# Kernel optimization log

Hardware: AMD Instinct MI355X
Metric: run time of the kernel (lower is better)

Reference implementation:

```python
import jax, jax.numpy as jnp
import numpy as np

N, E, G = 20000, 320000, 64
IN_CH, HID, HEADS = 128, 64, 8
LEAKY_SLOPE = 0.2
SOFTMAX_EPS = 1e-16


def setup_inputs() -> dict:
    key = jax.random.key(0)
    ks = jax.random.split(key, 12)
    s = lambda fan_in: 1.0 / np.sqrt(fan_in)
    return {
        "x": jax.random.normal(ks[0], (N, IN_CH), jnp.float32),
        "edge_index": jax.random.randint(ks[1], (2, E), 0, N, jnp.int32),
        "batch": jnp.sort(jax.random.randint(ks[2], (N,), 0, G, jnp.int32)),
        "W1": jax.random.normal(ks[3], (HEADS * HID, IN_CH), jnp.float32) * s(IN_CH),
        "att_src1": jax.random.normal(ks[4], (HEADS, HID), jnp.float32) * s(HID),
        "att_dst1": jax.random.normal(ks[5], (HEADS, HID), jnp.float32) * s(HID),
        "b1": jnp.zeros((HEADS * HID,), jnp.float32),
        "W2": jax.random.normal(ks[6], (HID, HEADS * HID), jnp.float32) * s(HEADS * HID),
        "att_src2": jax.random.normal(ks[7], (1, HID), jnp.float32) * s(HID),
        "att_dst2": jax.random.normal(ks[8], (1, HID), jnp.float32) * s(HID),
        "b2": jnp.zeros((HID,), jnp.float32),
    }


def gat_conv(x, src, dst, W, att_src, att_dst, b):
    # x: [N, F_in]; W: [H*C, F_in]; att_*: [H, C]; b: [H*C]
    n = x.shape[0]
    heads, ch = att_src.shape
    h = (x @ W.T).reshape(n, heads, ch)                    # [N,H,C]
    a_s = jnp.einsum('nhc,hc->nh', h, att_src)             # [N,H]
    a_d = jnp.einsum('nhc,hc->nh', h, att_dst)             # [N,H]
    e = jax.nn.leaky_relu(a_s[src] + a_d[dst], LEAKY_SLOPE)  # [E,H]
    m = jax.ops.segment_max(e, dst, num_segments=n)        # scatter-softmax (stable)
    e = jnp.exp(e - m[dst])
    z = jax.ops.segment_sum(e, dst, num_segments=n)
    alpha = e / (z[dst] + SOFTMAX_EPS)                     # [E,H]
    msg = h[src] * alpha[:, :, None]                       # [E,H,C]
    out = jax.ops.segment_sum(msg, dst, num_segments=n)    # [N,H,C]
    return out.reshape(n, heads * ch) + b


def reference(x, edge_index, batch, W1, att_src1, att_dst1, b1, W2, att_src2, att_dst2, b2):
    # PyG GATConv default: add self loops
    loop = jnp.arange(N, dtype=edge_index.dtype)
    src = jnp.concatenate([edge_index[0], loop])
    dst = jnp.concatenate([edge_index[1], loop])

    x_mid = jax.nn.relu(gat_conv(x, src, dst, W1, att_src1, att_dst1, b1))  # [N, H*C]

    # global_mean_pool over `batch` segments
    sums = jax.ops.segment_sum(x_mid, batch, num_segments=G)
    cnt = jax.ops.segment_sum(jnp.ones((N,), x_mid.dtype), batch, num_segments=G)
    gat_mid_pooled = sums / jnp.maximum(cnt, 1.0)[:, None]                  # [G, H*C]

    # dropout identity in eval mode
    x_late = gat_conv(x_mid, src, dst, W2, att_src2, att_dst2, b2)          # [N, C]
    gat_late_view = x_late.reshape(-1, HEADS * HID)                          # [N/H, H*C]
    return gat_mid_pooled, gat_late_view
```

## Files before the change

kernel.cpp:

```cpp
#include <hip/hip_runtime.h>
#include <math.h>

#define NN 20000
#define EE 320000
#define ETOT 340000
#define GG 64
#define INCH 128
#define HIDC 64
#define NH 8
#define HC 512
#define SLOPE 0.2f
#define SMEPS 1e-16f

typedef unsigned short u16;
typedef unsigned int u32;
typedef __attribute__((ext_vector_type(8))) short bf16x8;
typedef __attribute__((ext_vector_type(4))) float f32x4;
typedef __attribute__((ext_vector_type(2))) float f32x2;

__device__ __forceinline__ float rlanef(float v, int l) {
  return __uint_as_float(__builtin_amdgcn_readlane(__float_as_uint(v), l));
}
__device__ __forceinline__ u16 f2bf(float f) {
  u32 x = __float_as_uint(f);
  x += 0x7FFFu + ((x >> 16) & 1u);
  return (u16)(x >> 16);
}
__device__ __forceinline__ float bflo(u32 w) { return __uint_as_float(w << 16); }
__device__ __forceinline__ float bfhi(u32 w) { return __uint_as_float(w & 0xffff0000u); }

#define PREP_B 10392
#define HIST_B 1329
__global__ void k_prep(const float* __restrict__ W1, const float* __restrict__ W2,
                       const float* __restrict__ as1, const float* __restrict__ ad1v,
                       const float* __restrict__ x, const int* __restrict__ ei,
                       u16* __restrict__ W1bf, u16* __restrict__ W2bf,
                       float* __restrict__ wB1, u16* __restrict__ xbf,
                       int* __restrict__ deg) {
  if (blockIdx.x >= PREP_B) {
    int i = (blockIdx.x - PREP_B) * 256 + threadIdx.x;
    if (i < ETOT) {
      int d = (i < EE) ? ei[EE + i] : (i - EE);
      atomicAdd(&deg[d], 1);
    }
    return;
  }
  int i = blockIdx.x * 256 + threadIdx.x;
  if (i < 65536) {
    W1bf[i] = f2bf(W1[i]);
  } else if (i < 65536 + 32768) {
    int j = i - 65536;
    W2bf[j] = f2bf(W2[j]);
  } else if (i < 65536 + 32768 + 2048) {
    int j = i - 65536 - 32768;
    int k = j >> 4, c = j & 15;
    int h = c & 7;
    const float* av = (c < 8) ? as1 : ad1v;
    float s = 0.f;
    for (int q = 0; q < 64; ++q) s += W1[(h * 64 + q) * 128 + k] * av[h * 64 + q];
    wB1[j] = s;
  } else {
    int j = i - 100352;
    if (j < NN * INCH) xbf[j] = f2bf(x[j]);
  }
}

__global__ __launch_bounds__(1024) void k_scan(const int* __restrict__ deg,
                                               int* __restrict__ rowstart) {
  __shared__ int wtot[16];
  int tid = threadIdx.x;
  int lane = tid & 63, w = tid >> 6;
  int base = tid * 20;
  int v[20];
  int s = 0;
#pragma unroll
  for (int k = 0; k < 20; ++k) {
    v[k] = (base + k < NN) ? deg[base + k] : 0;
    s += v[k];
  }
  int ps = s;
#pragma unroll
  for (int off = 1; off < 64; off <<= 1) {
    int t = __shfl_up(ps, off);
    if (lane >= off) ps += t;
  }
  if (lane == 63) wtot[w] = ps;
  __syncthreads();
  if (w == 0 && lane < 16) {
    int t = wtot[lane];
#pragma unroll
    for (int off = 1; off < 16; off <<= 1) {
      int u = __shfl_up(t, off);
      if (lane >= off) t += u;
    }
    wtot[lane] = t;
  }
  __syncthreads();
  int woff = (w == 0) ? 0 : wtot[w - 1];
  int run = woff + ps - s;
#pragma unroll
  for (int k = 0; k < 20; ++k) {
    run += v[k];
    if (base + k < NN) rowstart[base + k + 1] = run;
  }
  if (tid == 0) rowstart[0] = 0;
}

__global__ void k_fill(const int* __restrict__ ei, const int* __restrict__ rowstart,
                       int* __restrict__ wcur, int* __restrict__ csr) {
  int i = blockIdx.x * 256 + threadIdx.x;
  if (i >= ETOT) return;
  int s, d;
  if (i < EE) { s = ei[i]; d = ei[EE + i]; } else { s = i - EE; d = s; }
  int pos = rowstart[d] + atomicAdd(&wcur[d], 1);
  csr[pos] = s;
}

__global__ __launch_bounds__(256) void k_logits1(
    const float* __restrict__ x, const float* __restrict__ wB1,
    float* __restrict__ al1) {
  __shared__ float bs[128][16];
  int tid = threadIdx.x;
#pragma unroll
  for (int i = 0; i < 8; ++i) {
    int e = tid + i * 256;
    bs[e >> 4][e & 15] = wB1[e];
  }
  __syncthreads();
  int gt = blockIdx.x * 256 + tid;
  int r = gt >> 2; if (r > NN - 1) r = NN - 1;
  int q = gt & 3;
  const float* xp = x + (size_t)r * INCH;
  float acc[4] = {0.f, 0.f, 0.f, 0.f};
  for (int kq = 0; kq < 32; ++kq) {
    float4 a = *(const float4*)(xp + kq * 4);
    float av[4] = {a.x, a.y, a.z, a.w};
#pragma unroll
    for (int kk = 0; kk < 4; ++kk) {
      const float4 b = *(const float4*)&bs[kq * 4 + kk][q * 4];
      acc[0] = fmaf(av[kk], b.x, acc[0]);
      acc[1] = fmaf(av[kk], b.y, acc[1]);
      acc[2] = fmaf(av[kk], b.z, acc[2]);
      acc[3] = fmaf(av[kk], b.w, acc[3]);
    }
  }
  float4 o; o.x = acc[0]; o.y = acc[1]; o.z = acc[2]; o.w = acc[3];
  *(float4*)(al1 + (size_t)r * 16 + q * 4) = o;
}

__global__ __launch_bounds__(256) void k_agg1(
    const u16* __restrict__ xbf, const float* __restrict__ al1,
    const int* __restrict__ rowstart, const int* __restrict__ csr,
    u16* __restrict__ aggbf) {
  int n = blockIdx.x * 4 + (threadIdx.x >> 6);
  int lane = threadIdx.x & 63;
  int rs = __builtin_amdgcn_readfirstlane(rowstart[n]);
  int re = __builtin_amdgcn_readfirstlane(rowstart[n + 1]);
  float4 ad0 = *(const float4*)(al1 + (size_t)n * 16 + 8);
  float4 ad1 = *(const float4*)(al1 + (size_t)n * 16 + 12);
  float zp[NH] = {};
  f32x2 acc2[NH] = {};
  for (int base = rs; base < re; base += 64) {
    int cn = min(64, re - base);
    int idx = base + ((lane < cn) ? lane : 0);
    int s = csr[idx];
    float4 a0 = *(const float4*)(al1 + (size_t)s * 16);
    float4 a1 = *(const float4*)(al1 + (size_t)s * 16 + 4);
    float e[8] = {a0.x + ad0.x, a0.y + ad0.y, a0.z + ad0.z, a0.w + ad0.w,
                  a1.x + ad1.x, a1.y + ad1.y, a1.z + ad1.z, a1.w + ad1.w};
    float p[8];
#pragma unroll
    for (int h = 0; h < 8; ++h) {
      float t = e[h];
      t = fmaxf(t, SLOPE * t);
      float pv = __expf(t);
      pv = (lane < cn) ? pv : 0.f;
      p[h] = pv;
      zp[h] += pv;
    }
    int j = 0;
    for (; j + 3 < cn; j += 4) {
      int s0 = __builtin_amdgcn_readlane(s, j);
      int s1 = __builtin_amdgcn_readlane(s, j + 1);
      int s2 = __builtin_amdgcn_readlane(s, j + 2);
      int s3 = __builtin_amdgcn_readlane(s, j + 3);
      u32 x0 = *(const u32*)(xbf + (size_t)s0 * INCH + lane * 2);
      u32 x1 = *(const u32*)(xbf + (size_t)s1 * INCH + lane * 2);
      u32 x2 = *(const u32*)(xbf + (size_t)s2 * INCH + lane * 2);
      u32 x3 = *(const u32*)(xbf + (size_t)s3 * INCH + lane * 2);
      f32x2 v0; v0.x = bflo(x0); v0.y = bfhi(x0);
      f32x2 v1; v1.x = bflo(x1); v1.y = bfhi(x1);
      f32x2 v2; v2.x = bflo(x2); v2.y = bfhi(x2);
      f32x2 v3; v3.x = bflo(x3); v3.y = bfhi(x3);
#pragma unroll
      for (int h = 0; h < 8; ++h) {
        float p0 = rlanef(p[h], j);
        float p1 = rlanef(p[h], j + 1);
        float p2 = rlanef(p[h], j + 2);
        float p3 = rlanef(p[h], j + 3);
        f32x2 q0; q0.x = p0; q0.y = p0;
        f32x2 q1; q1.x = p1; q1.y = p1;
        f32x2 q2; q2.x = p2; q2.y = p2;
        f32x2 q3; q3.x = p3; q3.y = p3;
        acc2[h] = __builtin_elementwise_fma(q0, v0, acc2[h]);
        acc2[h] = __builtin_elementwise_fma(q1, v1, acc2[h]);
        acc2[h] = __builtin_elementwise_fma(q2, v2, acc2[h]);
        acc2[h] = __builtin_elementwise_fma(q3, v3, acc2[h]);
      }
    }
    for (; j < cn; ++j) {
      int sa = __builtin_amdgcn_readlane(s, j);
      u32 xa = *(const u32*)(xbf + (size_t)sa * INCH + lane * 2);
      f32x2 va; va.x = bflo(xa); va.y = bfhi(xa);
#pragma unroll
      for (int h = 0; h < 8; ++h) {
        float pa = rlanef(p[h], j);
        f32x2 pa2; pa2.x = pa; pa2.y = pa;
        acc2[h] = __builtin_elementwise_fma(pa2, va, acc2[h]);
      }
    }
  }
#pragma unroll
  for (int h = 0; h < 8; ++h) {
    float z = zp[h];
#pragma unroll
    for (int off = 32; off; off >>= 1) z += __shfl_xor(z, off);
    float inv = 1.f / (z + SMEPS);
    u32 pk = ((u32)f2bf(acc2[h].y * inv) << 16) | (u32)f2bf(acc2[h].x * inv);
    *(u32*)(aggbf + (size_t)h * NN * INCH + (size_t)n * INCH + lane * 2) = pk;
  }
}

__global__ __launch_bounds__(256) void k_gemm1h(
    const u16* __restrict__ aggbf, const u16* __restrict__ W1bf,
    const float* __restrict__ b1, u16* __restrict__ xmidbf) {
  int tid = threadIdx.x;
  int head = blockIdx.x & 7;
  int nb = blockIdx.x >> 3;
  int w = tid >> 6, l = tid & 63;
  int li = l & 15, hi = l >> 4;
  const u16* Ab = aggbf + (size_t)head * NN * INCH;
  const u16* Bb = W1bf + (size_t)head * 64 * INCH;

  bf16x8 Bf[4][4];
#pragma unroll
  for (int ks = 0; ks < 4; ++ks)
#pragma unroll
    for (int ct = 0; ct < 4; ++ct)
      Bf[ks][ct] = *(const bf16x8*)(Bb + (size_t)(ct * 16 + li) * INCH + ks * 32 + hi * 8);

  int nA = nb * 64 + w * 16 + li; if (nA > NN - 1) nA = NN - 1;
  const u16* Ap = Ab + (size_t)nA * INCH + hi * 8;
  f32x4 acc[4] = {};
#pragma unroll
  for (int ks = 0; ks < 4; ++ks) {
    bf16x8 Af = *(const bf16x8*)(Ap + ks * 32);
#pragma unroll
    for (int ct = 0; ct < 4; ++ct)
      acc[ct] = __builtin_amdgcn_mfma_f32_16x16x32_bf16(Af, Bf[ks][ct], acc[ct], 0, 0, 0);
  }
#pragma unroll
  for (int ct = 0; ct < 4; ++ct) {
    float bb = b1[head * 64 + ct * 16 + li];
#pragma unroll
    for (int reg = 0; reg < 4; ++reg) {
      int r = nb * 64 + w * 16 + hi * 4 + reg; if (r > NN - 1) r = NN - 1;
      float v = fmaxf(acc[ct][reg] + bb, 0.f);
      xmidbf[(size_t)r * HC + head * 64 + ct * 16 + li] = f2bf(v);
    }
  }
}

__global__ __launch_bounds__(256) void k_gemm2(
    const u16* __restrict__ xmb, const u16* __restrict__ W2bf,
    const float* __restrict__ atts, const float* __restrict__ attd,
    u16* __restrict__ h2bf, float* __restrict__ as2, float* __restrict__ ad2) {
  __shared__ float red[4][16][65];
  int tid = threadIdx.x;
  int w = tid >> 6, l = tid & 63;
  int li = l & 15, hi = l >> 4;
  int brow = blockIdx.x * 16;

  bf16x8 Bf[4][4];
#pragma unroll
  for (int ksl = 0; ksl < 4; ++ksl)
#pragma unroll
    for (int ct = 0; ct < 4; ++ct)
      Bf[ksl][ct] = *(const bf16x8*)(W2bf + (size_t)(ct * 16 + li) * HC + w * 128 + ksl * 32 + hi * 8);

  const u16* Ap = xmb + (size_t)(brow + li) * HC + w * 128 + hi * 8;
  f32x4 acc[4] = {};
#pragma unroll
  for (int ksl = 0; ksl < 4; ++ksl) {
    bf16x8 Af = *(const bf16x8*)(Ap + ksl * 32);
#pragma unroll
    for (int ct = 0; ct < 4; ++ct)
      acc[ct] = __builtin_amdgcn_mfma_f32_16x16x32_bf16(Af, Bf[ksl][ct], acc[ct], 0, 0, 0);
  }
#pragma unroll
  for (int ct = 0; ct < 4; ++ct)
#pragma unroll
    for (int reg = 0; reg < 4; ++reg)
      red[w][hi * 4 + reg][ct * 16 + li] = acc[ct][reg];
  __syncthreads();

  int c = l;
  float atv = atts[c], adv = attd[c];
  float vs[4], vd[4];
#pragma unroll
  for (int i = 0; i < 4; ++i) {
    int r = w + 4 * i;
    float v = red[0][r][c] + red[1][r][c] + red[2][r][c] + red[3][r][c];
    h2bf[(size_t)(brow + r) * HIDC + c] = f2bf(v);
    vs[i] = v * atv; vd[i] = v * adv;
  }
#pragma unroll
  for (int off = 32; off; off >>= 1) {
#pragma unroll
    for (int i = 0; i < 4; ++i) { vs[i] += __shfl_xor(vs[i], off); vd[i] += __shfl_xor(vd[i], off); }
  }
  if (l == 0) {
#pragma unroll
    for (int i = 0; i < 4; ++i) {
      int n = brow + w + 4 * i;
      as2[n] = vs[i]; ad2[n] = vd[i];
    }
  }
}

__global__ __launch_bounds__(256) void k_node2(
    const u16* __restrict__ h2bf, const float* __restrict__ as2, const float* __restrict__ ad2,
    const int* __restrict__ rowstart, const int* __restrict__ csr,
    const float* __restrict__ b2, float* __restrict__ out) {
  int n = blockIdx.x * 4 + (threadIdx.x >> 6);
  int lane = threadIdx.x & 63;
  int e = lane >> 4, c = lane & 15;
  int rs = __builtin_amdgcn_readfirstlane(rowstart[n]);
  int re = __builtin_amdgcn_readfirstlane(rowstart[n + 1]);
  float ad = ad2[n];
  f32x2 accA = {}, accB = {};
  float zp = 0.f;
  for (int base = rs; base < re; base += 8) {
    int iA = base + e, iB = base + 4 + e;
    bool okA = iA < re, okB = iB < re;
    int sA = csr[okA ? iA : re - 1];
    int sB = csr[okB ? iB : re - 1];
    float tA = as2[sA] + ad;
    float tB = as2[sB] + ad;
    const u32* hpA = (const u32*)(h2bf + (size_t)sA * HIDC + c * 4);
    const u32* hpB = (const u32*)(h2bf + (size_t)sB * HIDC + c * 4);
    u32 a0 = hpA[0], a1 = hpA[1];
    u32 b0 = hpB[0], b1 = hpB[1];
    tA = fmaxf(tA, SLOPE * tA);
    tB = fmaxf(tB, SLOPE * tB);
    float pA = okA ? __expf(tA) : 0.f;
    float pB = okB ? __expf(tB) : 0.f;
    zp += pA + pB;
    f32x2 vA0; vA0.x = bflo(a0); vA0.y = bfhi(a0);
    f32x2 vA1; vA1.x = bflo(a1); vA1.y = bfhi(a1);
    f32x2 vB0; vB0.x = bflo(b0); vB0.y = bfhi(b0);
    f32x2 vB1; vB1.x = bflo(b1); vB1.y = bfhi(b1);
    f32x2 pA2; pA2.x = pA; pA2.y = pA;
    f32x2 pB2; pB2.x = pB; pB2.y = pB;
    accA = __builtin_elementwise_fma(pA2, vA0, accA);
    accB = __builtin_elementwise_fma(pA2, vA1, accB);
    accA = __builtin_elementwise_fma(pB2, vB0, accA);
    accB = __builtin_elementwise_fma(pB2, vB1, accB);
  }
  float acc0 = accA.x, acc1 = accA.y, acc2v = accB.x, acc3 = accB.y;
  zp += __shfl_xor(zp, 16); zp += __shfl_xor(zp, 32);
  acc0 += __shfl_xor(acc0, 16); acc0 += __shfl_xor(acc0, 32);
  acc1 += __shfl_xor(acc1, 16); acc1 += __shfl_xor(acc1, 32);
  acc2v += __shfl_xor(acc2v, 16); acc2v += __shfl_xor(acc2v, 32);
  acc3 += __shfl_xor(acc3, 16); acc3 += __shfl_xor(acc3, 32);
  if (e == 0) {
    float inv = 1.f / (zp + SMEPS);
    float4 bv = *(const float4*)(b2 + c * 4);
    float4 o;
    o.x = acc0 * inv + bv.x; o.y = acc1 * inv + bv.y;
    o.z = acc2v * inv + bv.z; o.w = acc3 * inv + bv.w;
    *(float4*)(out + (size_t)n * HIDC + c * 4) = o;
  }
}

__device__ inline int lowerb(const int* a, int n, int v) {
  int lo = 0, hi = n;
  while (lo < hi) { int mid = (lo + hi) >> 1; if (a[mid] < v) lo = mid + 1; else hi = mid; }
  return lo;
}

__global__ __launch_bounds__(256) void k_pool(const u16* __restrict__ xmb,
                                              const int* __restrict__ batch,
                                              float* __restrict__ out) {
  __shared__ float red[4][128];
  int g = blockIdx.x >> 2;
  int cb = blockIdx.x & 3;
  int tid = threadIdx.x;
  int c2 = tid & 63;
  int rq = tid >> 6;
  int lo = lowerb(batch, NN, g);
  int hi = lowerb(batch, NN, g + 1);
  float sx = 0.f, sy = 0.f;
  for (int n = lo + rq; n < hi; n += 4) {
    u32 w = *(const u32*)(xmb + (size_t)n * HC + cb * 128 + c2 * 2);
    sx += bflo(w); sy += bfhi(w);
  }
  red[rq][c2 * 2] = sx; red[rq][c2 * 2 + 1] = sy;
  __syncthreads();
  if (rq == 0) {
    float inv = 1.f / fmaxf((float)(hi - lo), 1.f);
    float vx = red[0][c2 * 2] + red[1][c2 * 2] + red[2][c2 * 2] + red[3][c2 * 2];
    float vy = red[0][c2 * 2 + 1] + red[1][c2 * 2 + 1] + red[2][c2 * 2 + 1] + red[3][c2 * 2 + 1];
    float2 o; o.x = vx * inv; o.y = vy * inv;
    *(float2*)(out + (size_t)g * HC + cb * 128 + c2 * 2) = o;
  }
}

extern "C" void kernel_launch(void* const* d_in, const int* in_sizes, int n_in,
                              void* d_out, int out_size, void* d_ws, size_t ws_size,
                              hipStream_t stream) {
  const float* x     = (const float*)d_in[0];
  const int*   ei    = (const int*)d_in[1];
  const int*   batch = (const int*)d_in[2];
  const float* W1    = (const float*)d_in[3];
  const float* atts1 = (const float*)d_in[4];
  const float* attd1 = (const float*)d_in[5];
  const float* b1    = (const float*)d_in[6];
  const float* W2    = (const float*)d_in[7];
  const float* atts2 = (const float*)d_in[8];
  const float* attd2 = (const float*)d_in[9];
  const float* b2    = (const float*)d_in[10];
  float* out = (float*)d_out;

  float* ws = (float*)d_ws;
  size_t off = 0;
  u16*  aggbf  = (u16*)(ws + off); off += (size_t)NH * NN * INCH / 2;
  u16*  xmidbf = (u16*)(ws + off); off += (size_t)NN * HC / 2;
  u16*  h2bf   = (u16*)(ws + off); off += (size_t)NN * HIDC / 2;
  float* al1  = ws + off; off += (size_t)NN * 16;
  float* as2  = ws + off; off += NN;
  float* ad2  = ws + off; off += NN;
  u16*  W1bf  = (u16*)(ws + off); off += 65536 / 2;
  u16*  W2bf  = (u16*)(ws + off); off += 32768 / 2;
  float* wB1  = ws + off; off += 2048;
  u16*  xbf   = (u16*)(ws + off); off += (size_t)NN * INCH / 2;
  int* deg      = (int*)(ws + off); off += NN;
  int* wcur     = (int*)(ws + off); off += NN;
  int* rowstart = (int*)(ws + off); off += NN + 4;
  int* csr      = (int*)(ws + off); off += ETOT;

  hipMemsetAsync(deg, 0, sizeof(int) * 2 * NN, stream);
  k_prep<<<PREP_B + HIST_B, 256, 0, stream>>>(W1, W2, atts1, attd1, x, ei,
                                              W1bf, W2bf, wB1, xbf, deg);
  k_scan<<<1, 1024, 0, stream>>>(deg, rowstart);
  k_fill<<<(ETOT + 255) / 256, 256, 0, stream>>>(ei, rowstart, wcur, csr);

  k_logits1<<<313, 256, 0, stream>>>(x, wB1, al1);
  k_agg1<<<5000, 256, 0, stream>>>(xbf, al1, rowstart, csr, aggbf);
  k_gemm1h<<<313 * 8, 256, 0, stream>>>(aggbf, W1bf, b1, xmidbf);
  k_pool<<<GG * 4, 256, 0, stream>>>(xmidbf, batch, out);
  k_gemm2<<<1250, 256, 0, stream>>>(xmidbf, W2bf, atts2, attd2, h2bf, as2, ad2);
  k_node2<<<5000, 256, 0, stream>>>(h2bf, as2, ad2, rowstart, csr, b2, out + (size_t)GG * HC);
}
```

Measured before the change: 188.1 us.

## Merge fill with logits and pool with gemm2; stage attention weights in LDS

The CSR fill kernel and the layer-1 logits kernel become one launch, with the blocks split by index. The mean-pool kernel is likewise folded into the layer-2 GEMM launch. Together these remove two kernel launches and let the independent work overlap. In the aggregation kernel, per-edge attention weights are written to shared memory and read back as vectors instead of being broadcast with readlane; this trades scalar readlane traffic for LDS reads and extra shared memory per block, which may reduce occupancy.

```diff
diff --git a/kernel.cpp b/kernel.cpp
--- a/kernel.cpp
+++ b/kernel.cpp
@@ -18,9 +18,6 @@
 typedef __attribute__((ext_vector_type(4))) float f32x4;
 typedef __attribute__((ext_vector_type(2))) float f32x2;
 
-__device__ __forceinline__ float rlanef(float v, int l) {
-  return __uint_as_float(__builtin_amdgcn_readlane(__float_as_uint(v), l));
-}
 __device__ __forceinline__ u16 f2bf(float f) {
   u32 x = __float_as_uint(f);
   x += 0x7FFFu + ((x >> 16) & 1u);
@@ -106,28 +103,30 @@
   if (tid == 0) rowstart[0] = 0;
 }
 
-__global__ void k_fill(const int* __restrict__ ei, const int* __restrict__ rowstart,
-                       int* __restrict__ wcur, int* __restrict__ csr) {
-  int i = blockIdx.x * 256 + threadIdx.x;
-  if (i >= ETOT) return;
-  int s, d;
-  if (i < EE) { s = ei[i]; d = ei[EE + i]; } else { s = i - EE; d = s; }
-  int pos = rowstart[d] + atomicAdd(&wcur[d], 1);
-  csr[pos] = s;
-}
-
-__global__ __launch_bounds__(256) void k_logits1(
+#define FILL_B 1329
+__global__ __launch_bounds__(256) void k_fill_logits(
+    const int* __restrict__ ei, const int* __restrict__ rowstart,
+    int* __restrict__ wcur, int* __restrict__ csr,
     const float* __restrict__ x, const float* __restrict__ wB1,
     float* __restrict__ al1) {
   __shared__ float bs[128][16];
   int tid = threadIdx.x;
+  if (blockIdx.x < FILL_B) {
+    int i = blockIdx.x * 256 + tid;
+    if (i >= ETOT) return;
+    int s, d;
+    if (i < EE) { s = ei[i]; d = ei[EE + i]; } else { s = i - EE; d = s; }
+    int pos = rowstart[d] + atomicAdd(&wcur[d], 1);
+    csr[pos] = s;
+    return;
+  }
 #pragma unroll
   for (int i = 0; i < 8; ++i) {
     int e = tid + i * 256;
     bs[e >> 4][e & 15] = wB1[e];
   }
   __syncthreads();
-  int gt = blockIdx.x * 256 + tid;
+  int gt = (blockIdx.x - FILL_B) * 256 + tid;
   int r = gt >> 2; if (r > NN - 1) r = NN - 1;
   int q = gt & 3;
   const float* xp = x + (size_t)r * INCH;
@@ -148,11 +147,14 @@
   *(float4*)(al1 + (size_t)r * 16 + q * 4) = o;
 }
 
+#define PSTR 12
 __global__ __launch_bounds__(256) void k_agg1(
     const u16* __restrict__ xbf, const float* __restrict__ al1,
     const int* __restrict__ rowstart, const int* __restrict__ csr,
     u16* __restrict__ aggbf) {
-  int n = blockIdx.x * 4 + (threadIdx.x >> 6);
+  __shared__ float p_sh[4][64 * PSTR];
+  int wv = threadIdx.x >> 6;
+  int n = blockIdx.x * 4 + wv;
   int lane = threadIdx.x & 63;
   int rs = __builtin_amdgcn_readfirstlane(rowstart[n]);
   int re = __builtin_amdgcn_readfirstlane(rowstart[n + 1]);
@@ -160,6 +162,7 @@
   float4 ad1 = *(const float4*)(al1 + (size_t)n * 16 + 12);
   float zp[NH] = {};
   f32x2 acc2[NH] = {};
+  float* pw = &p_sh[wv][0];
   for (int base = rs; base < re; base += 64) {
     int cn = min(64, re - base);
     int idx = base + ((lane < cn) ? lane : 0);
@@ -177,6 +180,13 @@
       pv = (lane < cn) ? pv : 0.f;
       p[h] = pv;
       zp[h] += pv;
+    }
+    {
+      float* pd = pw + lane * PSTR;
+      f32x4 w0; w0.x = p[0]; w0.y = p[1]; w0.z = p[2]; w0.w = p[3];
+      f32x4 w1; w1.x = p[4]; w1.y = p[5]; w1.z = p[6]; w1.w = p[7];
+      *(f32x4*)(pd) = w0;
+      *(f32x4*)(pd + 4) = w1;
     }
     int j = 0;
     for (; j + 3 < cn; j += 4) {
@@ -188,35 +198,56 @@
       u32 x1 = *(const u32*)(xbf + (size_t)s1 * INCH + lane * 2);
       u32 x2 = *(const u32*)(xbf + (size_t)s2 * INCH + lane * 2);
       u32 x3 = *(const u32*)(xbf + (size_t)s3 * INCH + lane * 2);
+      f32x4 pA0 = *(const f32x4*)(pw + (j + 0) * PSTR);
+      f32x4 pA1 = *(const f32x4*)(pw + (j + 0) * PSTR + 4);
+      f32x4 pB0 = *(const f32x4*)(pw + (j + 1) * PSTR);
+      f32x4 pB1 = *(const f32x4*)(pw + (j + 1) * PSTR + 4);
+      f32x4 pC0 = *(const f32x4*)(pw + (j + 2) * PSTR);
+      f32x4 pC1 = *(const f32x4*)(pw + (j + 2) * PSTR + 4);
+      f32x4 pD0 = *(const f32x4*)(pw + (j + 3) * PSTR);
+      f32x4 pD1 = *(const f32x4*)(pw + (j + 3) * PSTR + 4);
       f32x2 v0; v0.x = bflo(x0); v0.y = bfhi(x0);
       f32x2 v1; v1.x = bflo(x1); v1.y = bfhi(x1);
       f32x2 v2; v2.x = bflo(x2); v2.y = bfhi(x2);
       f32x2 v3; v3.x = bflo(x3); v3.y = bfhi(x3);
 #pragma unroll
-      for (int h = 0; h < 8; ++h) {
-        float p0 = rlanef(p[h], j);
-        float p1 = rlanef(p[h], j + 1);
-        float p2 = rlanef(p[h], j + 2);
-        float p3 = rlanef(p[h], j + 3);
-        f32x2 q0; q0.x = p0; q0.y = p0;
-        f32x2 q1; q1.x = p1; q1.y = p1;
-        f32x2 q2; q2.x = p2; q2.y = p2;
-        f32x2 q3; q3.x = p3; q3.y = p3;
-        acc2[h] = __builtin_elementwise_fma(q0, v0, acc2[h]);
-        acc2[h] = __builtin_elementwise_fma(q1, v1, acc2[h]);
-        acc2[h] = __builtin_elementwise_fma(q2, v2, acc2[h]);
-        acc2[h] = __builtin_elementwise_fma(q3, v3, acc2[h]);
+      for (int h = 0; h < 4; ++h) {
+        f32x2 qA; qA.x = pA0[h]; qA.y = pA0[h];
+        f32x2 qB; qB.x = pB0[h]; qB.y = pB0[h];
+        f32x2 qC; qC.x = pC0[h]; qC.y = pC0[h];
+        f32x2 qD; qD.x = pD0[h]; qD.y = pD0[h];
+        acc2[h] = __builtin_elementwise_fma(qA, v0, acc2[h]);
+        acc2[h] = __builtin_elementwise_fma(qB, v1, acc2[h]);
+        acc2[h] = __builtin_elementwise_fma(qC, v2, acc2[h]);
+        acc2[h] = __builtin_elementwise_fma(qD, v3, acc2[h]);
+      }
+#pragma unroll
+      for (int h = 0; h < 4; ++h) {
+        f32x2 qA; qA.x = pA1[h]; qA.y = pA1[h];
+        f32x2 qB; qB.x = pB1[h]; qB.y = pB1[h];
+        f32x2 qC; qC.x = pC1[h]; qC.y = pC1[h];
+        f32x2 qD; qD.x = pD1[h]; qD.y = pD1[h];
+        acc2[4 + h] = __builtin_elementwise_fma(qA, v0, acc2[4 + h]);
+        acc2[4 + h] = __builtin_elementwise_fma(qB, v1, acc2[4 + h]);
+        acc2[4 + h] = __builtin_elementwise_fma(qC, v2, acc2[4 + h]);
+        acc2[4 + h] = __builtin_elementwise_fma(qD, v3, acc2[4 + h]);
       }
     }
     for (; j < cn; ++j) {
       int sa = __builtin_amdgcn_readlane(s, j);
       u32 xa = *(const u32*)(xbf + (size_t)sa * INCH + lane * 2);
+      f32x4 pA0 = *(const f32x4*)(pw + j * PSTR);
+      f32x4 pA1 = *(const f32x4*)(pw + j * PSTR + 4);
       f32x2 va; va.x = bflo(xa); va.y = bfhi(xa);
 #pragma unroll
-      for (int h = 0; h < 8; ++h) {
-        float pa = rlanef(p[h], j);
-        f32x2 pa2; pa2.x = pa; pa2.y = pa;
-        acc2[h] = __builtin_elementwise_fma(pa2, va, acc2[h]);
+      for (int h = 0; h < 4; ++h) {
+        f32x2 qA; qA.x = pA0[h]; qA.y = pA0[h];
+        acc2[h] = __builtin_elementwise_fma(qA, va, acc2[h]);
+      }
+#pragma unroll
+      for (int h = 0; h < 4; ++h) {
+        f32x2 qA; qA.x = pA1[h]; qA.y = pA1[h];
+        acc2[4 + h] = __builtin_elementwise_fma(qA, va, acc2[4 + h]);
       }
     }
   }
@@ -271,12 +302,45 @@
   }
 }
 
-__global__ __launch_bounds__(256) void k_gemm2(
+#define G2_B 1250
+__device__ inline int lowerb(const int* a, int n, int v) {
+  int lo = 0, hi = n;
+  while (lo < hi) { int mid = (lo + hi) >> 1; if (a[mid] < v) lo = mid + 1; else hi = mid; }
+  return lo;
+}
+
+__global__ __launch_bounds__(256) void k_gemm2_pool(
     const u16* __restrict__ xmb, const u16* __restrict__ W2bf,
     const float* __restrict__ atts, const float* __restrict__ attd,
-    u16* __restrict__ h2bf, float* __restrict__ as2, float* __restrict__ ad2) {
+    u16* __restrict__ h2bf, float* __restrict__ as2, float* __restrict__ ad2,
+    const int* __restrict__ batch, float* __restrict__ out) {
   __shared__ float red[4][16][65];
+  __shared__ float redp[4][128];
   int tid = threadIdx.x;
+  if (blockIdx.x >= G2_B) {
+    int bid = blockIdx.x - G2_B;
+    int g = bid >> 2;
+    int cb = bid & 3;
+    int c2 = tid & 63;
+    int rq = tid >> 6;
+    int lo = lowerb(batch, NN, g);
+    int hi = lowerb(batch, NN, g + 1);
+    float sx = 0.f, sy = 0.f;
+    for (int n = lo + rq; n < hi; n += 4) {
+      u32 w = *(const u32*)(xmb + (size_t)n * HC + cb * 128 + c2 * 2);
+      sx += bflo(w); sy += bfhi(w);
+    }
+    redp[rq][c2 * 2] = sx; redp[rq][c2 * 2 + 1] = sy;
+    __syncthreads();
+    if (rq == 0) {
+      float inv = 1.f / fmaxf((float)(hi - lo), 1.f);
+      float vx = redp[0][c2 * 2] + redp[1][c2 * 2] + redp[2][c2 * 2] + redp[3][c2 * 2];
+      float vy = redp[0][c2 * 2 + 1] + redp[1][c2 * 2 + 1] + redp[2][c2 * 2 + 1] + redp[3][c2 * 2 + 1];
+      float2 o; o.x = vx * inv; o.y = vy * inv;
+      *(float2*)(out + (size_t)g * HC + cb * 128 + c2 * 2) = o;
+    }
+    return;
+  }
   int w = tid >> 6, l = tid & 63;
   int li = l & 15, hi = l >> 4;
   int brow = blockIdx.x * 16;
@@ -383,39 +447,6 @@
   }
 }
 
-__device__ inline int lowerb(const int* a, int n, int v) {
-  int lo = 0, hi = n;
-  while (lo < hi) { int mid = (lo + hi) >> 1; if (a[mid] < v) lo = mid + 1; else hi = mid; }
-  return lo;
-}
-
-__global__ __launch_bounds__(256) void k_pool(const u16* __restrict__ xmb,
-                                              const int* __restrict__ batch,
-                                              float* __restrict__ out) {
-  __shared__ float red[4][128];
-  int g = blockIdx.x >> 2;
-  int cb = blockIdx.x & 3;
-  int tid = threadIdx.x;
-  int c2 = tid & 63;
-  int rq = tid >> 6;
-  int lo = lowerb(batch, NN, g);
-  int hi = lowerb(batch, NN, g + 1);
-  float sx = 0.f, sy = 0.f;
-  for (int n = lo + rq; n < hi; n += 4) {
-    u32 w = *(const u32*)(xmb + (size_t)n * HC + cb * 128 + c2 * 2);
-    sx += bflo(w); sy += bfhi(w);
-  }
-  red[rq][c2 * 2] = sx; red[rq][c2 * 2 + 1] = sy;
-  __syncthreads();
-  if (rq == 0) {
-    float inv = 1.f / fmaxf((float)(hi - lo), 1.f);
-    float vx = red[0][c2 * 2] + red[1][c2 * 2] + red[2][c2 * 2] + red[3][c2 * 2];
-    float vy = red[0][c2 * 2 + 1] + red[1][c2 * 2 + 1] + red[2][c2 * 2 + 1] + red[3][c2 * 2 + 1];
-    float2 o; o.x = vx * inv; o.y = vy * inv;
-    *(float2*)(out + (size_t)g * HC + cb * 128 + c2 * 2) = o;
-  }
-}
-
 extern "C" void kernel_launch(void* const* d_in, const int* in_sizes, int n_in,
                               void* d_out, int out_size, void* d_ws, size_t ws_size,
                               hipStream_t stream) {
@@ -453,12 +484,10 @@
   k_prep<<<PREP_B + HIST_B, 256, 0, stream>>>(W1, W2, atts1, attd1, x, ei,
                                               W1bf, W2bf, wB1, xbf, deg);
   k_scan<<<1, 1024, 0, stream>>>(deg, rowstart);
-  k_fill<<<(ETOT + 255) / 256, 256, 0, stream>>>(ei, rowstart, wcur, csr);
-
-  k_logits1<<<313, 256, 0, stream>>>(x, wB1, al1);
+  k_fill_logits<<<FILL_B + 313, 256, 0, stream>>>(ei, rowstart, wcur, csr, x, wB1, al1);
   k_agg1<<<5000, 256, 0, stream>>>(xbf, al1, rowstart, csr, aggbf);
   k_gemm1h<<<313 * 8, 256, 0, stream>>>(aggbf, W1bf, b1, xmidbf);
-  k_pool<<<GG * 4, 256, 0, stream>>>(xmidbf, batch, out);
-  k_gemm2<<<1250, 256, 0, stream>>>(xmidbf, W2bf, atts2, attd2, h2bf, as2, ad2);
+  k_gemm2_pool<<<G2_B + GG * 4, 256, 0, stream>>>(xmidbf, W2bf, atts2, attd2,
+                                                  h2bf, as2, ad2, batch, out);
   k_node2<<<5000, 256, 0, stream>>>(h2bf, as2, ad2, rowstart, csr, b2, out + (size_t)GG * HC);
 }
```

New measurement: 179.0 us. 4.8% less time.
